# Performance work log

Hardware: AMD Instinct MI355X
Metric: run time of the kernel (lower is better)

Reference implementation:

```python
import jax, jax.numpy as jnp
import numpy as np
from jax import lax

INPUT_DIM = 64
HIDDEN = 128
NUM_CLASSES = 3


def _uniform(key, shape, scale):
    return jax.random.uniform(key, shape, jnp.float32, -scale, scale)


def setup_inputs() -> dict:
    key = jax.random.key(0)
    ks = jax.random.split(key, 16)
    s = 1.0 / np.sqrt(HIDDEN)
    inp = {
        "x": jax.random.normal(ks[0], (256, 512, INPUT_DIM), jnp.float32),
        # layer 0 LSTM params (PyTorch gate order: i, f, g, o)
        "W_ih0": _uniform(ks[1], (4 * HIDDEN, INPUT_DIM), s),
        "W_hh0": _uniform(ks[2], (4 * HIDDEN, HIDDEN), s),
        "b_ih0": _uniform(ks[3], (4 * HIDDEN,), s),
        "b_hh0": _uniform(ks[4], (4 * HIDDEN,), s),
        # layer 1 LSTM params
        "W_ih1": _uniform(ks[5], (4 * HIDDEN, HIDDEN), s),
        "W_hh1": _uniform(ks[6], (4 * HIDDEN, HIDDEN), s),
        "b_ih1": _uniform(ks[7], (4 * HIDDEN,), s),
        "b_hh1": _uniform(ks[8], (4 * HIDDEN,), s),
        # MLP head: fc1 (H -> H//2), fc2 (H//2 -> num_classes)
        "W1": _uniform(ks[9], (HIDDEN // 2, HIDDEN), s),
        "b1": _uniform(ks[10], (HIDDEN // 2,), s),
        "W2": _uniform(ks[11], (NUM_CLASSES, HIDDEN // 2), 1.0 / np.sqrt(HIDDEN // 2)),
        "b2": _uniform(ks[12], (NUM_CLASSES,), 1.0 / np.sqrt(HIDDEN // 2)),
    }
    return inp


def _lstm_layer(x, W_ih, W_hh, b_ih, b_hh):
    # x: [B, T, I] -> ys: [B, T, H]
    B = x.shape[0]
    H = W_hh.shape[1]
    b = b_ih + b_hh

    def step(carry, xt):
        h, c = carry
        g = xt @ W_ih.T + h @ W_hh.T + b  # [B, 4H]
        i, f, gg, o = jnp.split(g, 4, axis=-1)
        c = jax.nn.sigmoid(f) * c + jax.nn.sigmoid(i) * jnp.tanh(gg)
        h = jax.nn.sigmoid(o) * jnp.tanh(c)
        return (h, c), h

    h0 = jnp.zeros((B, H), x.dtype)
    (_, _), ys = lax.scan(step, (h0, h0), jnp.swapaxes(x, 0, 1))
    return jnp.swapaxes(ys, 0, 1)


def reference(x, W_ih0, W_hh0, b_ih0, b_hh0, W_ih1, W_hh1, b_ih1, b_hh1, W1, b1, W2, b2):
    # Eval mode: dropout layers are identity.
    h = _lstm_layer(x, W_ih0, W_hh0, b_ih0, b_hh0)   # [B, T, H]
    h = _lstm_layer(h, W_ih1, W_hh1, b_ih1, b_hh1)   # [B, T, H]
    last = h[:, -1, :]                                # [B, H]
    out = jax.nn.relu(last @ W1.T + b1) @ W2.T + b2   # [B, num_classes]
    return out
```

## Files before the change

kernel.cpp:

```cpp
#include <hip/hip_runtime.h>
#include <hip/hip_bf16.h>
#include <stdint.h>

#define BATCH 256
#define SEQ   512
#define INDIM 64
#define H     128
#define RB    4
#define NTILE (BATCH / RB)
#define CH    16
#define NCH   (SEQ / CH)

using short8  = __attribute__((ext_vector_type(8))) short;
using float4v = __attribute__((ext_vector_type(4))) float;

#define LOG2E 1.4426950408889634f

__device__ __forceinline__ unsigned short f2bf(float f) {
    union { float f; uint32_t u; } v; v.f = f;
    uint32_t u = v.u;
    return (unsigned short)((u + 0x7FFFu + ((u >> 16) & 1u)) >> 16);
}

__device__ __forceinline__ float fast_exp2(float x) {
#if __has_builtin(__builtin_amdgcn_exp2f)
    return __builtin_amdgcn_exp2f(x);
#else
    return __expf(x * 0.6931471805599453f);
#endif
}
__device__ __forceinline__ float fast_rcp(float x) {
#if __has_builtin(__builtin_amdgcn_rcpf)
    return __builtin_amdgcn_rcpf(x);
#else
    return 1.f / x;
#endif
}
__device__ __forceinline__ float sigmoid_fast(float x) {
    return fast_rcp(1.f + fast_exp2(-LOG2E * x));
}
__device__ __forceinline__ float tanh_fast(float x) {
    return fmaf(-2.f, fast_rcp(1.f + fast_exp2((2.f * LOG2E) * x)), 1.f);
}

__device__ __forceinline__ void light_barrier() {
    asm volatile("s_waitcnt lgkmcnt(0)\n\ts_barrier" ::: "memory");
}

__global__ void conv_x_kernel(const float* __restrict__ x,
                              unsigned short* __restrict__ xb, int n4,
                              int* __restrict__ flags) {
    int i = blockIdx.x * blockDim.x + threadIdx.x;
    if (blockIdx.x == 0 && threadIdx.x < NTILE) flags[threadIdx.x] = 0;
    if (i >= n4) return;
    float4 f = ((const float4*)x)[i];
    ushort4 o;
    o.x = f2bf(f.x); o.y = f2bf(f.y); o.z = f2bf(f.z); o.w = f2bf(f.w);
    ((ushort4*)xb)[i] = o;
}

template<int KIN, bool IS_PROD>
__device__ __forceinline__ void lstm_body(
    const unsigned short* __restrict__ xin,
    const float* __restrict__ Wih,
    const float* __restrict__ Whh,
    const float* __restrict__ b_ih, const float* __restrict__ b_hh,
    unsigned short* __restrict__ outseq,
    const float* __restrict__ W1, const float* __restrict__ b1,
    const float* __restrict__ W2, const float* __restrict__ b2,
    float* __restrict__ out,
    int* flag, int bt)
{
    constexpr int KT  = KIN / 32;
    constexpr int PAD = 132;
    const int lane = threadIdx.x & 63;
    const int quad = lane >> 4;
    const int l16  = lane & 15;
    const int b0   = bt * RB;
    const int cell = (threadIdx.x >> 6) * 16 + l16;
    const int arow = l16 & 12;
    const int xrow = b0 + (l16 >> 2);

    __shared__ short hbuf[2][16][PAD];
    __shared__ float hl[RB][128];
    __shared__ float mid[RB][65];
    for (int i = threadIdx.x; i < 2 * 16 * PAD; i += 512) ((short*)hbuf)[i] = 0;

    short8 whh_f[4][4];
    short8 wih_f[4][KT];
    float  bias[4];
#pragma unroll
    for (int tT = 0; tT < 4; tT++) {
        const int n = tT * 128 + cell;
#pragma unroll
        for (int kt = 0; kt < 4; kt++) {
            const float* p = Whh + (size_t)n * H + kt * 32 + quad * 8;
            float4 f0 = *(const float4*)p;
            float4 f1 = *(const float4*)(p + 4);
            short8 s;
            s[0]=f2bf(f0.x); s[1]=f2bf(f0.y); s[2]=f2bf(f0.z); s[3]=f2bf(f0.w);
            s[4]=f2bf(f1.x); s[5]=f2bf(f1.y); s[6]=f2bf(f1.z); s[7]=f2bf(f1.w);
            whh_f[tT][kt] = s;
        }
#pragma unroll
        for (int kt = 0; kt < KT; kt++) {
            const float* p = Wih + (size_t)n * KIN + kt * 32 + quad * 8;
            float4 f0 = *(const float4*)p;
            float4 f1 = *(const float4*)(p + 4);
            short8 s;
            s[0]=f2bf(f0.x); s[1]=f2bf(f0.y); s[2]=f2bf(f0.z); s[3]=f2bf(f0.w);
            s[4]=f2bf(f1.x); s[5]=f2bf(f1.y); s[6]=f2bf(f1.z); s[7]=f2bf(f1.w);
            wih_f[tT][kt] = s;
        }
        bias[tT] = b_ih[n] + b_hh[n];
    }

    float c0 = 0.f;

    const unsigned short* xp = xin + ((size_t)xrow * SEQ) * KIN + quad * 8;
    unsigned short* op = nullptr;
    if (IS_PROD)
        op = outseq + ((size_t)(b0 + quad) * SEQ) * H + cell;

    short8 xf0[KT], xf1[KT];
    __syncthreads();

    auto step = [&](int t, int CUR, short8 (&xf)[KT],
                    bool doPre) __attribute__((always_inline)) {
        short8 ha[4];
#pragma unroll
        for (int kt = 0; kt < 4; kt++)
            ha[kt] = *(const short8*)&hbuf[CUR][arow][kt * 32 + quad * 8];

        float4v accA[4], accB[4];
#pragma unroll
        for (int tT = 0; tT < 4; tT++) {
            accA[tT] = (float4v){bias[tT], bias[tT], bias[tT], bias[tT]};
            accB[tT] = (float4v){0.f, 0.f, 0.f, 0.f};
        }
#pragma unroll
        for (int tT = 0; tT < 4; tT++)
            accA[tT] = __builtin_amdgcn_mfma_f32_16x16x32_bf16(xf[0], wih_f[tT][0], accA[tT], 0, 0, 0);
#pragma unroll
        for (int tT = 0; tT < 4; tT++)
            accA[tT] = __builtin_amdgcn_mfma_f32_16x16x32_bf16(xf[1], wih_f[tT][1], accA[tT], 0, 0, 0);
        if constexpr (KT == 4) {
#pragma unroll
            for (int tT = 0; tT < 4; tT++)
                accB[tT] = __builtin_amdgcn_mfma_f32_16x16x32_bf16(xf[2], wih_f[tT][2], accB[tT], 0, 0, 0);
#pragma unroll
            for (int tT = 0; tT < 4; tT++)
                accB[tT] = __builtin_amdgcn_mfma_f32_16x16x32_bf16(xf[3], wih_f[tT][3], accB[tT], 0, 0, 0);
        }
        if (doPre) {
            const unsigned short* p = xp + (size_t)(t + 2) * KIN;
#pragma unroll
            for (int kt = 0; kt < KT; kt++) xf[kt] = *(const short8*)(p + kt * 32);
        }
#pragma unroll
        for (int tT = 0; tT < 4; tT++)
            accA[tT] = __builtin_amdgcn_mfma_f32_16x16x32_bf16(ha[0], whh_f[tT][0], accA[tT], 0, 0, 0);
#pragma unroll
        for (int tT = 0; tT < 4; tT++)
            accB[tT] = __builtin_amdgcn_mfma_f32_16x16x32_bf16(ha[2], whh_f[tT][2], accB[tT], 0, 0, 0);
#pragma unroll
        for (int tT = 0; tT < 4; tT++)
            accA[tT] = __builtin_amdgcn_mfma_f32_16x16x32_bf16(ha[1], whh_f[tT][1], accA[tT], 0, 0, 0);
#pragma unroll
        for (int tT = 0; tT < 4; tT++)
            accB[tT] = __builtin_amdgcn_mfma_f32_16x16x32_bf16(ha[3], whh_f[tT][3], accB[tT], 0, 0, 0);

        float g0 = accA[0][0] + accB[0][0];
        float g1 = accA[1][0] + accB[1][0];
        float g2 = accA[2][0] + accB[2][0];
        float g3 = accA[3][0] + accB[3][0];

        float si = sigmoid_fast(g0);
        float sf = sigmoid_fast(g1);
        float tg = tanh_fast(g2);
        float so = sigmoid_fast(g3);
        c0 = fmaf(sf, c0, si * tg);
        float h = so * tanh_fast(c0);
        uint32_t hp;
        asm("v_cvt_pk_bf16_f32 %0, %1, %2" : "=v"(hp) : "v"(h), "v"(h));
        hbuf[CUR ^ 1][quad * 4][cell] = (short)(hp & 0xffffu);
        if (IS_PROD) {
            *op = (unsigned short)(hp & 0xffffu);
            op += H;
        } else if (t == SEQ - 1) {
            hl[quad][cell] = h;
        }
        light_barrier();
    };

    for (int ch = 0; ch < NCH; ch++) {
        const int t0 = ch * CH;
        if (!IS_PROD) {
            if (threadIdx.x == 0) {
                while (__hip_atomic_load(flag, __ATOMIC_RELAXED, __HIP_MEMORY_SCOPE_AGENT) <= ch)
                    __builtin_amdgcn_s_sleep(2);
                (void)__hip_atomic_load(flag, __ATOMIC_ACQUIRE, __HIP_MEMORY_SCOPE_AGENT);
            }
            __syncthreads();
        }
        if (!IS_PROD || ch == 0) {
            const unsigned short* p0 = xp + (size_t)t0 * KIN;
            const unsigned short* p1 = p0 + KIN;
#pragma unroll
            for (int kt = 0; kt < KT; kt++) {
                xf0[kt] = *(const short8*)(p0 + kt * 32);
                xf1[kt] = *(const short8*)(p1 + kt * 32);
            }
        }

#pragma unroll 1
        for (int i = 0; i < CH; i += 2) {
            const int t = t0 + i;
            const bool pre0 = IS_PROD ? (t + 2 < SEQ) : (i + 2 < CH);
            const bool pre1 = IS_PROD ? (t + 3 < SEQ) : (i + 3 < CH);
            step(t,     0, xf0, pre0);
            step(t + 1, 1, xf1, pre1);
        }
        __syncthreads();
        if (IS_PROD && threadIdx.x == 0)
            __hip_atomic_fetch_add(flag, 1, __ATOMIC_RELEASE, __HIP_MEMORY_SCOPE_AGENT);
    }

    if (!IS_PROD) {
        if (threadIdx.x < RB * 64) {
            const int row = threadIdx.x >> 6, j = threadIdx.x & 63;
            float s = b1[j];
            const float* wr = W1 + (size_t)j * 128;
#pragma unroll 8
            for (int k = 0; k < 128; k++) s = fmaf(hl[row][k], wr[k], s);
            mid[row][j] = fmaxf(s, 0.f);
        }
        __syncthreads();
        if (threadIdx.x < RB * 3) {
            const int row = threadIdx.x / 3, k = threadIdx.x - row * 3;
            float o = b2[k];
            const float* wr = W2 + (size_t)k * 64;
#pragma unroll 8
            for (int j = 0; j < 64; j++) o = fmaf(mid[row][j], wr[j], o);
            out[(size_t)(b0 + row) * 3 + k] = o;
        }
    }
}

__global__ __launch_bounds__(512, 2)
void lstm_fused_kernel(const unsigned short* __restrict__ xb,
                       const float* __restrict__ Wih0, const float* __restrict__ Whh0,
                       const float* __restrict__ bih0, const float* __restrict__ bhh0,
                       const float* __restrict__ Wih1, const float* __restrict__ Whh1,
                       const float* __restrict__ bih1, const float* __restrict__ bhh1,
                       unsigned short* __restrict__ h0sq,
                       const float* __restrict__ W1, const float* __restrict__ b1,
                       const float* __restrict__ W2, const float* __restrict__ b2,
                       float* __restrict__ out,
                       int* __restrict__ flags)
{
    const int bt = blockIdx.x & (NTILE - 1);
    if (blockIdx.x < NTILE)
        lstm_body<64,  true >(xb,   Wih0, Whh0, bih0, bhh0, h0sq,
                              W1, b1, W2, b2, out, flags + bt, bt);
    else
        lstm_body<128, false>(h0sq, Wih1, Whh1, bih1, bhh1, nullptr,
                              W1, b1, W2, b2, out, flags + bt, bt);
}

extern "C" void kernel_launch(void* const* d_in, const int* in_sizes, int n_in,
                              void* d_out, int out_size, void* d_ws, size_t ws_size,
                              hipStream_t stream) {
    const float* x     = (const float*)d_in[0];
    const float* W_ih0 = (const float*)d_in[1];
    const float* W_hh0 = (const float*)d_in[2];
    const float* b_ih0 = (const float*)d_in[3];
    const float* b_hh0 = (const float*)d_in[4];
    const float* W_ih1 = (const float*)d_in[5];
    const float* W_hh1 = (const float*)d_in[6];
    const float* b_ih1 = (const float*)d_in[7];
    const float* b_hh1 = (const float*)d_in[8];
    const float* W1    = (const float*)d_in[9];
    const float* b1    = (const float*)d_in[10];
    const float* W2    = (const float*)d_in[11];
    const float* b2    = (const float*)d_in[12];
    float* out = (float*)d_out;

    char* ws = (char*)d_ws;
    unsigned short* xb    = (unsigned short*)ws;
    unsigned short* h0sq  = (unsigned short*)(ws + 16777216);
    int*            flags = (int*)(ws + 50331648);

    conv_x_kernel<<<8192, 256, 0, stream>>>(x, xb, (BATCH * SEQ * INDIM) / 4, flags);
    lstm_fused_kernel<<<2 * NTILE, 512, 0, stream>>>(xb, W_ih0, W_hh0, b_ih0, b_hh0,
                                                     W_ih1, W_hh1, b_ih1, b_hh1,
                                                     h0sq, W1, b1, W2, b2, out, flags);
}
```

Before: 472.6 us.

## Split LSTM gate accumulators four ways and loosen layer-1 producer wait

The gate MFMA chain now uses four independent accumulator sets instead of two, which shortens the dependent MFMA chain on the recurrent critical path. The consumer (layer-1) now spins per-thread, waits until the producer is two chunks ahead, and no longer uses a block-wide barrier or a chunk reload. It prefetches one step ahead with a single register buffer instead of two steps ahead. This cuts barrier overhead and the stalls of the cross-layer handoff, at the cost of more accumulator registers and every thread polling the flag.

Result: slower. 543.6 us (+15.0%).

```diff
diff --git a/kernel.cpp b/kernel.cpp
--- a/kernel.cpp
+++ b/kernel.cpp
@@ -72,6 +72,7 @@
     int* flag, int bt)
 {
     constexpr int KT  = KIN / 32;
+    constexpr int PD  = IS_PROD ? 2 : 1;
     constexpr int PAD = 132;
     const int lane = threadIdx.x & 63;
     const int quad = lane >> 4;
@@ -132,48 +133,50 @@
         for (int kt = 0; kt < 4; kt++)
             ha[kt] = *(const short8*)&hbuf[CUR][arow][kt * 32 + quad * 8];
 
-        float4v accA[4], accB[4];
+        float4v accA[4], accB[4], accC[4], accD[4];
 #pragma unroll
         for (int tT = 0; tT < 4; tT++) {
             accA[tT] = (float4v){bias[tT], bias[tT], bias[tT], bias[tT]};
             accB[tT] = (float4v){0.f, 0.f, 0.f, 0.f};
+            accC[tT] = (float4v){0.f, 0.f, 0.f, 0.f};
+            accD[tT] = (float4v){0.f, 0.f, 0.f, 0.f};
         }
 #pragma unroll
         for (int tT = 0; tT < 4; tT++)
             accA[tT] = __builtin_amdgcn_mfma_f32_16x16x32_bf16(xf[0], wih_f[tT][0], accA[tT], 0, 0, 0);
 #pragma unroll
         for (int tT = 0; tT < 4; tT++)
-            accA[tT] = __builtin_amdgcn_mfma_f32_16x16x32_bf16(xf[1], wih_f[tT][1], accA[tT], 0, 0, 0);
+            accB[tT] = __builtin_amdgcn_mfma_f32_16x16x32_bf16(xf[1], wih_f[tT][1], accB[tT], 0, 0, 0);
         if constexpr (KT == 4) {
 #pragma unroll
             for (int tT = 0; tT < 4; tT++)
-                accB[tT] = __builtin_amdgcn_mfma_f32_16x16x32_bf16(xf[2], wih_f[tT][2], accB[tT], 0, 0, 0);
+                accA[tT] = __builtin_amdgcn_mfma_f32_16x16x32_bf16(xf[2], wih_f[tT][2], accA[tT], 0, 0, 0);
 #pragma unroll
             for (int tT = 0; tT < 4; tT++)
                 accB[tT] = __builtin_amdgcn_mfma_f32_16x16x32_bf16(xf[3], wih_f[tT][3], accB[tT], 0, 0, 0);
         }
         if (doPre) {
-            const unsigned short* p = xp + (size_t)(t + 2) * KIN;
+            const unsigned short* p = xp + (size_t)(t + PD) * KIN;
 #pragma unroll
             for (int kt = 0; kt < KT; kt++) xf[kt] = *(const short8*)(p + kt * 32);
         }
 #pragma unroll
         for (int tT = 0; tT < 4; tT++)
+            accC[tT] = __builtin_amdgcn_mfma_f32_16x16x32_bf16(ha[2], whh_f[tT][2], accC[tT], 0, 0, 0);
+#pragma unroll
+        for (int tT = 0; tT < 4; tT++)
+            accD[tT] = __builtin_amdgcn_mfma_f32_16x16x32_bf16(ha[3], whh_f[tT][3], accD[tT], 0, 0, 0);
+#pragma unroll
+        for (int tT = 0; tT < 4; tT++)
             accA[tT] = __builtin_amdgcn_mfma_f32_16x16x32_bf16(ha[0], whh_f[tT][0], accA[tT], 0, 0, 0);
 #pragma unroll
         for (int tT = 0; tT < 4; tT++)
-            accB[tT] = __builtin_amdgcn_mfma_f32_16x16x32_bf16(ha[2], whh_f[tT][2], accB[tT], 0, 0, 0);
-#pragma unroll
-        for (int tT = 0; tT < 4; tT++)
-            accA[tT] = __builtin_amdgcn_mfma_f32_16x16x32_bf16(ha[1], whh_f[tT][1], accA[tT], 0, 0, 0);
-#pragma unroll
-        for (int tT = 0; tT < 4; tT++)
-            accB[tT] = __builtin_amdgcn_mfma_f32_16x16x32_bf16(ha[3], whh_f[tT][3], accB[tT], 0, 0, 0);
-
-        float g0 = accA[0][0] + accB[0][0];
-        float g1 = accA[1][0] + accB[1][0];
-        float g2 = accA[2][0] + accB[2][0];
-        float g3 = accA[3][0] + accB[3][0];
+            accB[tT] = __builtin_amdgcn_mfma_f32_16x16x32_bf16(ha[1], whh_f[tT][1], accB[tT], 0, 0, 0);
+
+        float g0 = (accA[0][0] + accB[0][0]) + (accC[0][0] + accD[0][0]);
+        float g1 = (accA[1][0] + accB[1][0]) + (accC[1][0] + accD[1][0]);
+        float g2 = (accA[2][0] + accB[2][0]) + (accC[2][0] + accD[2][0]);
+        float g3 = (accA[3][0] + accB[3][0]) + (accC[3][0] + accD[3][0]);
 
         float si = sigmoid_fast(g0);
         float sf = sigmoid_fast(g1);
@@ -196,34 +199,37 @@
     for (int ch = 0; ch < NCH; ch++) {
         const int t0 = ch * CH;
         if (!IS_PROD) {
-            if (threadIdx.x == 0) {
-                while (__hip_atomic_load(flag, __ATOMIC_RELAXED, __HIP_MEMORY_SCOPE_AGENT) <= ch)
-                    __builtin_amdgcn_s_sleep(2);
-                (void)__hip_atomic_load(flag, __ATOMIC_ACQUIRE, __HIP_MEMORY_SCOPE_AGENT);
-            }
-            __syncthreads();
-        }
-        if (!IS_PROD || ch == 0) {
-            const unsigned short* p0 = xp + (size_t)t0 * KIN;
-            const unsigned short* p1 = p0 + KIN;
-#pragma unroll
-            for (int kt = 0; kt < KT; kt++) {
-                xf0[kt] = *(const short8*)(p0 + kt * 32);
-                xf1[kt] = *(const short8*)(p1 + kt * 32);
+            const int want = (ch + 2 < NCH) ? (ch + 2) : NCH;
+            while (__hip_atomic_load(flag, __ATOMIC_RELAXED, __HIP_MEMORY_SCOPE_AGENT) < want)
+                __builtin_amdgcn_s_sleep(2);
+            (void)__hip_atomic_load(flag, __ATOMIC_ACQUIRE, __HIP_MEMORY_SCOPE_AGENT);
+        }
+        if (ch == 0) {
+            const unsigned short* p0 = xp;
+#pragma unroll
+            for (int kt = 0; kt < KT; kt++) xf0[kt] = *(const short8*)(p0 + kt * 32);
+            if constexpr (IS_PROD) {
+#pragma unroll
+                for (int kt = 0; kt < KT; kt++) xf1[kt] = *(const short8*)(p0 + KIN + kt * 32);
             }
         }
 
 #pragma unroll 1
         for (int i = 0; i < CH; i += 2) {
             const int t = t0 + i;
-            const bool pre0 = IS_PROD ? (t + 2 < SEQ) : (i + 2 < CH);
-            const bool pre1 = IS_PROD ? (t + 3 < SEQ) : (i + 3 < CH);
-            step(t,     0, xf0, pre0);
-            step(t + 1, 1, xf1, pre1);
-        }
-        __syncthreads();
-        if (IS_PROD && threadIdx.x == 0)
-            __hip_atomic_fetch_add(flag, 1, __ATOMIC_RELEASE, __HIP_MEMORY_SCOPE_AGENT);
+            if constexpr (IS_PROD) {
+                step(t,     0, xf0, t + PD     < SEQ);
+                step(t + 1, 1, xf1, t + 1 + PD < SEQ);
+            } else {
+                step(t,     0, xf0, t + PD     < SEQ);
+                step(t + 1, 1, xf0, t + 1 + PD < SEQ);
+            }
+        }
+        if constexpr (IS_PROD) {
+            __syncthreads();
+            if (threadIdx.x == 0)
+                __hip_atomic_fetch_add(flag, 1, __ATOMIC_RELEASE, __HIP_MEMORY_SCOPE_AGENT);
+        }
     }
 
     if (!IS_PROD) {
```

## Halve LSTM block size, each thread computes two hidden cells

Applied to the files above, without the earlier changes.

Each block now runs 256 threads (4 waves) instead of 512, and every lane handles two hidden cells, so it holds twice the bf16 weight fragments in registers and issues twice as many MFMAs per step. The aim is to cut the per-timestep barrier cost and the number of waves synchronising on the serial recurrence, and to interleave two independent accumulator chains for more MFMA ILP. In exchange, register pressure roughly doubles (launch bounds relaxed to 256,1), so spills or lower occupancy are possible, and each wave does more serial work per step.

Result: slower. 556.8 us (+17.8%).

```diff
diff --git a/kernel.cpp b/kernel.cpp
--- a/kernel.cpp
+++ b/kernel.cpp
@@ -77,45 +77,55 @@
     const int quad = lane >> 4;
     const int l16  = lane & 15;
     const int b0   = bt * RB;
-    const int cell = (threadIdx.x >> 6) * 16 + l16;
+    const int cell = (threadIdx.x >> 6) * 32 + l16;
     const int arow = l16 & 12;
     const int xrow = b0 + (l16 >> 2);
 
     __shared__ short hbuf[2][16][PAD];
     __shared__ float hl[RB][128];
     __shared__ float mid[RB][65];
-    for (int i = threadIdx.x; i < 2 * 16 * PAD; i += 512) ((short*)hbuf)[i] = 0;
-
-    short8 whh_f[4][4];
-    short8 wih_f[4][KT];
-    float  bias[4];
+    for (int i = threadIdx.x; i < 2 * 16 * PAD; i += 256) ((short*)hbuf)[i] = 0;
+
+    short8 whh_f[4][4], whh_g[4][4];
+    short8 wih_f[4][KT], wih_g[4][KT];
+    float  biasA[4], biasB[4];
 #pragma unroll
     for (int tT = 0; tT < 4; tT++) {
-        const int n = tT * 128 + cell;
+        const int n0 = tT * 128 + cell;
+        const int n1 = n0 + 16;
 #pragma unroll
         for (int kt = 0; kt < 4; kt++) {
-            const float* p = Whh + (size_t)n * H + kt * 32 + quad * 8;
-            float4 f0 = *(const float4*)p;
-            float4 f1 = *(const float4*)(p + 4);
-            short8 s;
-            s[0]=f2bf(f0.x); s[1]=f2bf(f0.y); s[2]=f2bf(f0.z); s[3]=f2bf(f0.w);
-            s[4]=f2bf(f1.x); s[5]=f2bf(f1.y); s[6]=f2bf(f1.z); s[7]=f2bf(f1.w);
-            whh_f[tT][kt] = s;
+            const float* p0 = Whh + (size_t)n0 * H + kt * 32 + quad * 8;
+            const float* p1 = Whh + (size_t)n1 * H + kt * 32 + quad * 8;
+            float4 a0 = *(const float4*)p0, a1 = *(const float4*)(p0 + 4);
+            float4 c0v = *(const float4*)p1, c1v = *(const float4*)(p1 + 4);
+            short8 s0, s1;
+            s0[0]=f2bf(a0.x); s0[1]=f2bf(a0.y); s0[2]=f2bf(a0.z); s0[3]=f2bf(a0.w);
+            s0[4]=f2bf(a1.x); s0[5]=f2bf(a1.y); s0[6]=f2bf(a1.z); s0[7]=f2bf(a1.w);
+            s1[0]=f2bf(c0v.x); s1[1]=f2bf(c0v.y); s1[2]=f2bf(c0v.z); s1[3]=f2bf(c0v.w);
+            s1[4]=f2bf(c1v.x); s1[5]=f2bf(c1v.y); s1[6]=f2bf(c1v.z); s1[7]=f2bf(c1v.w);
+            whh_f[tT][kt] = s0;
+            whh_g[tT][kt] = s1;
         }
 #pragma unroll
         for (int kt = 0; kt < KT; kt++) {
-            const float* p = Wih + (size_t)n * KIN + kt * 32 + quad * 8;
-            float4 f0 = *(const float4*)p;
-            float4 f1 = *(const float4*)(p + 4);
-            short8 s;
-            s[0]=f2bf(f0.x); s[1]=f2bf(f0.y); s[2]=f2bf(f0.z); s[3]=f2bf(f0.w);
-            s[4]=f2bf(f1.x); s[5]=f2bf(f1.y); s[6]=f2bf(f1.z); s[7]=f2bf(f1.w);
-            wih_f[tT][kt] = s;
-        }
-        bias[tT] = b_ih[n] + b_hh[n];
+            const float* p0 = Wih + (size_t)n0 * KIN + kt * 32 + quad * 8;
+            const float* p1 = Wih + (size_t)n1 * KIN + kt * 32 + quad * 8;
+            float4 a0 = *(const float4*)p0, a1 = *(const float4*)(p0 + 4);
+            float4 c0v = *(const float4*)p1, c1v = *(const float4*)(p1 + 4);
+            short8 s0, s1;
+            s0[0]=f2bf(a0.x); s0[1]=f2bf(a0.y); s0[2]=f2bf(a0.z); s0[3]=f2bf(a0.w);
+            s0[4]=f2bf(a1.x); s0[5]=f2bf(a1.y); s0[6]=f2bf(a1.z); s0[7]=f2bf(a1.w);
+            s1[0]=f2bf(c0v.x); s1[1]=f2bf(c0v.y); s1[2]=f2bf(c0v.z); s1[3]=f2bf(c0v.w);
+            s1[4]=f2bf(c1v.x); s1[5]=f2bf(c1v.y); s1[6]=f2bf(c1v.z); s1[7]=f2bf(c1v.w);
+            wih_f[tT][kt] = s0;
+            wih_g[tT][kt] = s1;
+        }
+        biasA[tT] = b_ih[n0] + b_hh[n0];
+        biasB[tT] = b_ih[n1] + b_hh[n1];
     }
 
-    float c0 = 0.f;
+    float cs0 = 0.f, cs1 = 0.f;
 
     const unsigned short* xp = xin + ((size_t)xrow * SEQ) * KIN + quad * 8;
     unsigned short* op = nullptr;
@@ -132,25 +142,35 @@
         for (int kt = 0; kt < 4; kt++)
             ha[kt] = *(const short8*)&hbuf[CUR][arow][kt * 32 + quad * 8];
 
-        float4v accA[4], accB[4];
-#pragma unroll
-        for (int tT = 0; tT < 4; tT++) {
-            accA[tT] = (float4v){bias[tT], bias[tT], bias[tT], bias[tT]};
-            accB[tT] = (float4v){0.f, 0.f, 0.f, 0.f};
-        }
-#pragma unroll
-        for (int tT = 0; tT < 4; tT++)
-            accA[tT] = __builtin_amdgcn_mfma_f32_16x16x32_bf16(xf[0], wih_f[tT][0], accA[tT], 0, 0, 0);
-#pragma unroll
-        for (int tT = 0; tT < 4; tT++)
-            accA[tT] = __builtin_amdgcn_mfma_f32_16x16x32_bf16(xf[1], wih_f[tT][1], accA[tT], 0, 0, 0);
+        float4v aA0[4], aB0[4], aA1[4], aB1[4];
+#pragma unroll
+        for (int tT = 0; tT < 4; tT++) {
+            aA0[tT] = (float4v){biasA[tT], biasA[tT], biasA[tT], biasA[tT]};
+            aA1[tT] = (float4v){biasB[tT], biasB[tT], biasB[tT], biasB[tT]};
+            aB0[tT] = (float4v){0.f, 0.f, 0.f, 0.f};
+            aB1[tT] = (float4v){0.f, 0.f, 0.f, 0.f};
+        }
+#pragma unroll
+        for (int tT = 0; tT < 4; tT++) {
+            aA0[tT] = __builtin_amdgcn_mfma_f32_16x16x32_bf16(xf[0], wih_f[tT][0], aA0[tT], 0, 0, 0);
+            aA1[tT] = __builtin_amdgcn_mfma_f32_16x16x32_bf16(xf[0], wih_g[tT][0], aA1[tT], 0, 0, 0);
+        }
+#pragma unroll
+        for (int tT = 0; tT < 4; tT++) {
+            aA0[tT] = __builtin_amdgcn_mfma_f32_16x16x32_bf16(xf[1], wih_f[tT][1], aA0[tT], 0, 0, 0);
+            aA1[tT] = __builtin_amdgcn_mfma_f32_16x16x32_bf16(xf[1], wih_g[tT][1], aA1[tT], 0, 0, 0);
+        }
         if constexpr (KT == 4) {
 #pragma unroll
-            for (int tT = 0; tT < 4; tT++)
-                accB[tT] = __builtin_amdgcn_mfma_f32_16x16x32_bf16(xf[2], wih_f[tT][2], accB[tT], 0, 0, 0);
-#pragma unroll
-            for (int tT = 0; tT < 4; tT++)
-                accB[tT] = __builtin_amdgcn_mfma_f32_16x16x32_bf16(xf[3], wih_f[tT][3], accB[tT], 0, 0, 0);
+            for (int tT = 0; tT < 4; tT++) {
+                aB0[tT] = __builtin_amdgcn_mfma_f32_16x16x32_bf16(xf[2], wih_f[tT][2], aB0[tT], 0, 0, 0);
+                aB1[tT] = __builtin_amdgcn_mfma_f32_16x16x32_bf16(xf[2], wih_g[tT][2], aB1[tT], 0, 0, 0);
+            }
+#pragma unroll
+            for (int tT = 0; tT < 4; tT++) {
+                aB0[tT] = __builtin_amdgcn_mfma_f32_16x16x32_bf16(xf[3], wih_f[tT][3], aB0[tT], 0, 0, 0);
+                aB1[tT] = __builtin_amdgcn_mfma_f32_16x16x32_bf16(xf[3], wih_g[tT][3], aB1[tT], 0, 0, 0);
+            }
         }
         if (doPre) {
             const unsigned short* p = xp + (size_t)(t + 2) * KIN;
@@ -158,37 +178,56 @@
             for (int kt = 0; kt < KT; kt++) xf[kt] = *(const short8*)(p + kt * 32);
         }
 #pragma unroll
-        for (int tT = 0; tT < 4; tT++)
-            accA[tT] = __builtin_amdgcn_mfma_f32_16x16x32_bf16(ha[0], whh_f[tT][0], accA[tT], 0, 0, 0);
-#pragma unroll
-        for (int tT = 0; tT < 4; tT++)
-            accB[tT] = __builtin_amdgcn_mfma_f32_16x16x32_bf16(ha[2], whh_f[tT][2], accB[tT], 0, 0, 0);
-#pragma unroll
-        for (int tT = 0; tT < 4; tT++)
-            accA[tT] = __builtin_amdgcn_mfma_f32_16x16x32_bf16(ha[1], whh_f[tT][1], accA[tT], 0, 0, 0);
-#pragma unroll
-        for (int tT = 0; tT < 4; tT++)
-            accB[tT] = __builtin_amdgcn_mfma_f32_16x16x32_bf16(ha[3], whh_f[tT][3], accB[tT], 0, 0, 0);
-
-        float g0 = accA[0][0] + accB[0][0];
-        float g1 = accA[1][0] + accB[1][0];
-        float g2 = accA[2][0] + accB[2][0];
-        float g3 = accA[3][0] + accB[3][0];
-
-        float si = sigmoid_fast(g0);
-        float sf = sigmoid_fast(g1);
-        float tg = tanh_fast(g2);
-        float so = sigmoid_fast(g3);
-        c0 = fmaf(sf, c0, si * tg);
-        float h = so * tanh_fast(c0);
+        for (int tT = 0; tT < 4; tT++) {
+            aA0[tT] = __builtin_amdgcn_mfma_f32_16x16x32_bf16(ha[0], whh_f[tT][0], aA0[tT], 0, 0, 0);
+            aA1[tT] = __builtin_amdgcn_mfma_f32_16x16x32_bf16(ha[0], whh_g[tT][0], aA1[tT], 0, 0, 0);
+        }
+#pragma unroll
+        for (int tT = 0; tT < 4; tT++) {
+            aB0[tT] = __builtin_amdgcn_mfma_f32_16x16x32_bf16(ha[2], whh_f[tT][2], aB0[tT], 0, 0, 0);
+            aB1[tT] = __builtin_amdgcn_mfma_f32_16x16x32_bf16(ha[2], whh_g[tT][2], aB1[tT], 0, 0, 0);
+        }
+#pragma unroll
+        for (int tT = 0; tT < 4; tT++) {
+            aA0[tT] = __builtin_amdgcn_mfma_f32_16x16x32_bf16(ha[1], whh_f[tT][1], aA0[tT], 0, 0, 0);
+            aA1[tT] = __builtin_amdgcn_mfma_f32_16x16x32_bf16(ha[1], whh_g[tT][1], aA1[tT], 0, 0, 0);
+        }
+#pragma unroll
+        for (int tT = 0; tT < 4; tT++) {
+            aB0[tT] = __builtin_amdgcn_mfma_f32_16x16x32_bf16(ha[3], whh_f[tT][3], aB0[tT], 0, 0, 0);
+            aB1[tT] = __builtin_amdgcn_mfma_f32_16x16x32_bf16(ha[3], whh_g[tT][3], aB1[tT], 0, 0, 0);
+        }
+
+        float g00 = aA0[0][0] + aB0[0][0];
+        float g01 = aA0[1][0] + aB0[1][0];
+        float g02 = aA0[2][0] + aB0[2][0];
+        float g03 = aA0[3][0] + aB0[3][0];
+        float g10 = aA1[0][0] + aB1[0][0];
+        float g11 = aA1[1][0] + aB1[1][0];
+        float g12 = aA1[2][0] + aB1[2][0];
+        float g13 = aA1[3][0] + aB1[3][0];
+
+        float si0 = sigmoid_fast(g00), si1 = sigmoid_fast(g10);
+        float sf0 = sigmoid_fast(g01), sf1 = sigmoid_fast(g11);
+        float tg0 = tanh_fast(g02),    tg1 = tanh_fast(g12);
+        float so0 = sigmoid_fast(g03), so1 = sigmoid_fast(g13);
+        cs0 = fmaf(sf0, cs0, si0 * tg0);
+        cs1 = fmaf(sf1, cs1, si1 * tg1);
+        float h0 = so0 * tanh_fast(cs0);
+        float h1 = so1 * tanh_fast(cs1);
         uint32_t hp;
-        asm("v_cvt_pk_bf16_f32 %0, %1, %2" : "=v"(hp) : "v"(h), "v"(h));
-        hbuf[CUR ^ 1][quad * 4][cell] = (short)(hp & 0xffffu);
+        asm("v_cvt_pk_bf16_f32 %0, %1, %2" : "=v"(hp) : "v"(h0), "v"(h1));
+        const unsigned short lo = (unsigned short)(hp & 0xffffu);
+        const unsigned short hi = (unsigned short)(hp >> 16);
+        hbuf[CUR ^ 1][quad * 4][cell]      = (short)lo;
+        hbuf[CUR ^ 1][quad * 4][cell + 16] = (short)hi;
         if (IS_PROD) {
-            *op = (unsigned short)(hp & 0xffffu);
+            op[0]  = lo;
+            op[16] = hi;
             op += H;
         } else if (t == SEQ - 1) {
-            hl[quad][cell] = h;
+            hl[quad][cell]      = h0;
+            hl[quad][cell + 16] = h1;
         }
         light_barrier();
     };
@@ -227,7 +266,7 @@
     }
 
     if (!IS_PROD) {
-        if (threadIdx.x < RB * 64) {
+        {
             const int row = threadIdx.x >> 6, j = threadIdx.x & 63;
             float s = b1[j];
             const float* wr = W1 + (size_t)j * 128;
@@ -247,7 +286,7 @@
     }
 }
 
-__global__ __launch_bounds__(512, 2)
+__global__ __launch_bounds__(256, 1)
 void lstm_fused_kernel(const unsigned short* __restrict__ xb,
                        const float* __restrict__ Wih0, const float* __restrict__ Whh0,
                        const float* __restrict__ bih0, const float* __restrict__ bhh0,
@@ -292,7 +331,7 @@
     int*            flags = (int*)(ws + 50331648);
 
     conv_x_kernel<<<8192, 256, 0, stream>>>(x, xb, (BATCH * SEQ * INDIM) / 4, flags);
-    lstm_fused_kernel<<<2 * NTILE, 512, 0, stream>>>(xb, W_ih0, W_hh0, b_ih0, b_hh0,
+    lstm_fused_kernel<<<2 * NTILE, 256, 0, stream>>>(xb, W_ih0, W_hh0, b_ih0, b_hh0,
                                                      W_ih1, W_hh1, b_ih1, b_hh1,
                                                      h0sq, W1, b1, W2, b2, out, flags);
 }
```
